# Kernel tuning notes

Measured on AMD Instinct MI355X. Metric: run time of the kernel, lower is better.

Reference implementation:

```python
import jax, jax.numpy as jnp
import numpy as np

DIM = 768
HEAD_DIM = 768


def setup_inputs() -> dict:
    key = jax.random.key(0)
    k_x, k_w, k_b = jax.random.split(key, 3)
    x = jax.random.normal(k_x, (4, 4096, DIM), dtype=jnp.float32)
    # torch Linear(dim, 3*head_dim): weight [3H, dim]; store transposed [dim, 3H]
    scale = 1.0 / np.sqrt(DIM)
    W_qkv = jax.random.uniform(k_w, (DIM, 3 * HEAD_DIM), dtype=jnp.float32,
                               minval=-scale, maxval=scale)
    b_qkv = jax.random.uniform(k_b, (3 * HEAD_DIM,), dtype=jnp.float32,
                               minval=-scale, maxval=scale)
    return {"x": x, "W_qkv": W_qkv, "b_qkv": b_qkv}


def reference(x, W_qkv, b_qkv):
    # x: [B, N, C]
    qkv = jnp.einsum("bnc,ch->bnh", x, W_qkv) + b_qkv  # [B, N, 3H]
    q, k, v = jnp.split(qkv, 3, axis=-1)               # each [B, N, H]
    H = q.shape[-1]
    scores = jnp.einsum("bnh,bmh->bnm", q, k) / jnp.sqrt(jnp.float32(H))
    attn = jax.nn.softmax(scores, axis=-1)             # [B, N, N]
    out = jnp.einsum("bnm,bmh->bnh", attn, v)          # [B, N, H]
    return out
```

## Files before the change

### kernel.cpp

```cpp
#include <hip/hip_runtime.h>
#include <stdint.h>

typedef __attribute__((ext_vector_type(8))) short short8;
typedef __attribute__((ext_vector_type(4))) float f32x4;

#define DIM 768
#define H3 2304
#define SEQ 4096
#define NTOK 16384

__device__ __forceinline__ unsigned short f2bf(float f) {
  union { float f; uint32_t u; } c; c.f = f;
  uint32_t u = c.u;
  u += 0x7FFFu + ((u >> 16) & 1u);
  return (unsigned short)(u >> 16);
}

__device__ __forceinline__ void async_cp16(const void* g, void* l) {
  __builtin_amdgcn_global_load_lds(
      (__attribute__((address_space(1))) void*)(void*)g,
      (__attribute__((address_space(3))) void*)l, 16, 0, 0);
}

#define MEMFENCE() asm volatile("" ::: "memory")
#define BARRIER() do { MEMFENCE(); __builtin_amdgcn_s_barrier(); MEMFENCE(); } while (0)
#define WAIT_VMCNT(n) asm volatile("s_waitcnt vmcnt(" #n ")" ::: "memory")

template <int N>
__device__ __forceinline__ void wait_lgk() {
  asm volatile("s_waitcnt lgkmcnt(%0)" :: "n"(N) : "memory");
  __builtin_amdgcn_sched_barrier(0);
}

template<int JN>
__device__ __forceinline__ void gemm_nt64_t(
    const unsigned short* __restrict__ A, const unsigned short* __restrict__ B,
    int K, int ldA, int ldB,
    unsigned short* As, unsigned short* Bs, f32x4 acc[4][JN])
{
  const int tid = threadIdx.x, lane = tid & 63, wid = tid >> 6;
  const int wm = (wid & 1) << 6, wn = (wid >> 1) * (JN * 16);
  const int lr = lane & 15, q = lane >> 4;

#pragma unroll
  for (int i = 0; i < 4; ++i)
#pragma unroll
    for (int j = 0; j < JN; ++j)
      acc[i][j] = (f32x4){0.f, 0.f, 0.f, 0.f};

  const unsigned short* gA[4];
  const unsigned short* gB[JN];
#pragma unroll
  for (int t = 0; t < 4; ++t) {
    const int c = tid + 256 * t;
    const int row = c >> 3, sc = c & 7;
    gA[t] = A + (size_t)row * ldA + (((sc ^ (row & 7)) << 3));
  }
#pragma unroll
  for (int t = 0; t < JN; ++t) {
    const int c = tid + 256 * t;
    const int row = c >> 3, sc = c & 7;
    gB[t] = B + (size_t)row * ldB + (((sc ^ (row & 7)) << 3));
  }

  for (int k0 = 0; k0 < K; k0 += 64) {
#pragma unroll
    for (int t = 0; t < 4; ++t)
      async_cp16(gA[t] + k0, As + (tid + 256 * t) * 8);
#pragma unroll
    for (int t = 0; t < JN; ++t)
      async_cp16(gB[t] + k0, Bs + (tid + 256 * t) * 8);
    __syncthreads();

    short8 af[4][2], bfr[JN][2];
#pragma unroll
    for (int i = 0; i < 4; ++i) {
      const int ra = wm + i * 16 + lr;
#pragma unroll
      for (int s2 = 0; s2 < 2; ++s2)
        af[i][s2] = *(const short8*)(As + ra * 64 + (((s2 * 4 + q) ^ (ra & 7)) << 3));
    }
#pragma unroll
    for (int j = 0; j < JN; ++j) {
      const int rb = wn + j * 16 + lr;
#pragma unroll
      for (int s2 = 0; s2 < 2; ++s2)
        bfr[j][s2] = *(const short8*)(Bs + rb * 64 + (((s2 * 4 + q) ^ (rb & 7)) << 3));
    }
#pragma unroll
    for (int s2 = 0; s2 < 2; ++s2)
#pragma unroll
      for (int i = 0; i < 4; ++i)
#pragma unroll
        for (int j = 0; j < JN; ++j)
          acc[i][j] = __builtin_amdgcn_mfma_f32_16x16x32_bf16(af[i][s2], bfr[j][s2], acc[i][j], 0, 0, 0);
    __syncthreads();
  }
}

template<int JN>
__device__ __forceinline__ void gemm256_nt(
    const unsigned short* __restrict__ A, const unsigned short* __restrict__ B,
    int K, int ldA, int ldB, unsigned short* lds, f32x4 acc[8][JN])
{
  constexpr int NB = JN - 2;
  const int tid = threadIdx.x, lane = tid & 63, wid = tid >> 6;
  const int wr = wid >> 2, wc = wid & 3;
  const int lr = lane & 15, q = lane >> 4;

  unsigned short* const As0 = lds;
  unsigned short* const As1 = lds + 16384;
  unsigned short* const Bs0 = lds + 32768;
  unsigned short* const Bs1 = lds + 32768 + JN * 4096;

#pragma unroll
  for (int i = 0; i < 8; ++i)
#pragma unroll
    for (int j = 0; j < JN; ++j)
      acc[i][j] = (f32x4){0.f, 0.f, 0.f, 0.f};

  const unsigned short* gA[4];
  const unsigned short* gB[JN];
#pragma unroll
  for (int t = 0; t < 4; ++t) {
    const int c = tid + 512 * t, row = c >> 3, sc = c & 7;
    gA[t] = A + (size_t)row * ldA + ((sc ^ (row & 7)) << 3);
  }
#pragma unroll
  for (int t = 0; t < JN; ++t) {
    const int c = tid + 512 * t, row = c >> 3, sc = c & 7;
    gB[t] = B + (size_t)row * ldB + ((sc ^ (row & 7)) << 3);
  }

  unsigned offA[8][2], offB[JN][2];
#pragma unroll
  for (int i = 0; i < 8; ++i) {
    const int ra = wr * 128 + i * 16 + lr;
#pragma unroll
    for (int h = 0; h < 2; ++h)
      offA[i][h] = ra * 64 + (((h * 4 + q) ^ (ra & 7)) << 3);
  }
#pragma unroll
  for (int j = 0; j < JN; ++j) {
    const int rb = wc * (JN * 16) + j * 16 + lr;
#pragma unroll
    for (int h = 0; h < 2; ++h)
      offB[j][h] = rb * 64 + (((h * 4 + q) ^ (rb & 7)) << 3);
  }

  const int nt = K >> 6;

#pragma unroll
  for (int t = 0; t < 4; ++t) async_cp16(gA[t], As0 + (tid + 512 * t) * 8);
#pragma unroll
  for (int t = 0; t < JN; ++t) async_cp16(gB[t], Bs0 + (tid + 512 * t) * 8);
  const int k1 = (nt > 1) ? 64 : 0;
#pragma unroll
  for (int t = 0; t < 4; ++t) async_cp16(gA[t] + k1, As1 + (tid + 512 * t) * 8);
  WAIT_VMCNT(4);
  BARRIER();

#pragma unroll 2
  for (int t = 0; t < nt; ++t) {
    const int p = t & 1;
    const unsigned short* const Asp = p ? As1 : As0;
    const unsigned short* const Bsp = p ? Bs1 : Bs0;
    unsigned short* const Bsn = p ? Bs0 : Bs1;
    unsigned short* const Asn = p ? As1 : As0;
    const int kB = ((t + 1 < nt) ? t + 1 : nt - 1) << 6;
    const int kA = ((t + 2 < nt) ? t + 2 : nt - 1) << 6;

#pragma unroll
    for (int u = 0; u < JN; ++u)
      async_cp16(gB[u] + kB, Bsn + (tid + 512 * u) * 8);

    short8 fa0[8], fa1[8], fbj[2], fbk[(NB > 0) ? NB : 1];
#pragma unroll
    for (int i = 0; i < 8; ++i) fa0[i] = *(const short8*)(Asp + offA[i][0]);
#pragma unroll
    for (int j = 0; j < 2; ++j) fbj[j] = *(const short8*)(Bsp + offB[j][0]);
#pragma unroll
    for (int j = 0; j < NB; ++j) fbk[j] = *(const short8*)(Bsp + offB[2 + j][0]);

    wait_lgk<NB>();
    __builtin_amdgcn_s_setprio(1);
#pragma unroll
    for (int i = 0; i < 8; ++i)
#pragma unroll
      for (int j = 0; j < 2; ++j)
        acc[i][j] = __builtin_amdgcn_mfma_f32_16x16x32_bf16(fa0[i], fbj[j], acc[i][j], 0, 0, 0);
    __builtin_amdgcn_s_setprio(0);

#pragma unroll
    for (int i = 0; i < 8; ++i) fa1[i] = *(const short8*)(Asp + offA[i][1]);
#pragma unroll
    for (int j = 0; j < 2; ++j) fbj[j] = *(const short8*)(Bsp + offB[j][1]);

    wait_lgk<10>();
    __builtin_amdgcn_s_setprio(1);
#pragma unroll
    for (int i = 0; i < 8; ++i)
#pragma unroll
      for (int j = 0; j < NB; ++j)
        acc[i][2 + j] = __builtin_amdgcn_mfma_f32_16x16x32_bf16(fa0[i], fbk[j], acc[i][2 + j], 0, 0, 0);
    __builtin_amdgcn_s_setprio(0);

#pragma unroll
    for (int j = 0; j < NB; ++j) fbk[j] = *(const short8*)(Bsp + offB[2 + j][1]);

    wait_lgk<NB>();
    __builtin_amdgcn_s_setprio(1);
#pragma unroll
    for (int i = 0; i < 8; ++i)
#pragma unroll
      for (int j = 0; j < 2; ++j)
        acc[i][j] = __builtin_amdgcn_mfma_f32_16x16x32_bf16(fa1[i], fbj[j], acc[i][j], 0, 0, 0);
    __builtin_amdgcn_s_setprio(0);

    BARRIER();
#pragma unroll
    for (int u = 0; u < 4; ++u)
      async_cp16(gA[u] + kA, Asn + (tid + 512 * u) * 8);

    wait_lgk<0>();
    __builtin_amdgcn_s_setprio(1);
#pragma unroll
    for (int i = 0; i < 8; ++i)
#pragma unroll
      for (int j = 0; j < NB; ++j)
        acc[i][2 + j] = __builtin_amdgcn_mfma_f32_16x16x32_bf16(fa1[i], fbk[j], acc[i][2 + j], 0, 0, 0);
    __builtin_amdgcn_s_setprio(0);

    WAIT_VMCNT(4);
    BARRIER();
  }
  WAIT_VMCNT(0);
  BARRIER();
}

__global__ __launch_bounds__(256) void k_cvt(const float* __restrict__ in,
                                             unsigned short* __restrict__ o) {
  int i = blockIdx.x * 256 + threadIdx.x;
  float4 f = ((const float4*)in)[i];
  ushort4 u;
  u.x = f2bf(f.x); u.y = f2bf(f.y); u.z = f2bf(f.z); u.w = f2bf(f.w);
  ((ushort4*)o)[i] = u;
}

__global__ __launch_bounds__(256) void k_transpose(const float* __restrict__ W,
                                                   unsigned short* __restrict__ Wt) {
  __shared__ float tile[32][33];
  const int bc = blockIdx.x * 32;
  const int br = blockIdx.y * 32;
  const int tx = threadIdx.x & 31, ty = threadIdx.x >> 5;
#pragma unroll
  for (int i = 0; i < 32; i += 8)
    tile[ty + i][tx] = W[(size_t)(br + ty + i) * H3 + bc + tx];
  __syncthreads();
#pragma unroll
  for (int i = 0; i < 32; i += 8)
    Wt[(size_t)(bc + ty + i) * DIM + br + tx] = f2bf(tile[tx][ty + i]);
}

__global__ __launch_bounds__(256) void k_qkv(
    const unsigned short* __restrict__ xbf, const unsigned short* __restrict__ Wt,
    const float* __restrict__ bias,
    unsigned short* __restrict__ qb, unsigned short* __restrict__ kb,
    unsigned short* __restrict__ vT)
{
  __shared__ unsigned short As[128 * 64];
  __shared__ unsigned short Bs[128 * 64];
  f32x4 acc[4][4];
  const int g = blockIdx.x;
  const int xcd = g & 7, slot = g >> 3;
  const int tn = slot % 18, grp = slot / 18;
  const int tm = xcd + 8 * grp;
  gemm_nt64_t<4>(xbf + (size_t)(tm * 128) * DIM, Wt + (size_t)(tn * 128) * DIM,
                 DIM, DIM, DIM, As, Bs, acc);

  const int tid = threadIdx.x, lane = tid & 63, wid = tid >> 6;
  const int wm = (wid & 1) << 6, wn = (wid >> 1) << 6;
  const float scale = 0.036084391824351615f;
#pragma unroll
  for (int i = 0; i < 4; ++i) {
#pragma unroll
    for (int j = 0; j < 4; ++j) {
      const int col  = tn * 128 + wn + j * 16 + (lane & 15);
      const int row0 = tm * 128 + wm + i * 16 + ((lane >> 4) << 2);
      const float bc = bias[col];
#pragma unroll
      for (int r = 0; r < 4; ++r) {
        const int row = row0 + r;
        const float v = acc[i][j][r] + bc;
        if (col < 768) {
          qb[(size_t)row * DIM + col] = f2bf(v * scale);
        } else if (col < 1536) {
          kb[(size_t)row * DIM + (col - 768)] = f2bf(v);
        } else {
          const int b = row >> 12, n = row & 4095;
          vT[((size_t)b * DIM + (col - 1536)) * SEQ + n] = f2bf(v);
        }
      }
    }
  }
}

__global__ __launch_bounds__(512, 2) void k_scores(
    const unsigned short* __restrict__ qb, const unsigned short* __restrict__ kb,
    unsigned short* __restrict__ S, float* __restrict__ lpart)
{
  __shared__ unsigned short lds[65536];
  f32x4 acc[8][4];
  const int g = blockIdx.x;
  const int xcd = g & 7, slot = g >> 3;
  const int grp = slot & 7, tn = slot >> 3;
  const int b  = xcd >> 1;
  const int ty = (grp << 1) | (xcd & 1);
  gemm256_nt<4>(qb + ((size_t)b * SEQ + ty * 256) * DIM,
                kb + ((size_t)b * SEQ + tn * 256) * DIM,
                DIM, DIM, DIM, lds, acc);

  const int tid = threadIdx.x, lane = tid & 63, wid = tid >> 6;
  const int wr = wid >> 2, wc = wid & 3;
  const int lr = lane & 15, q = lane >> 4;

  float rs[8][4];
#pragma unroll
  for (int i = 0; i < 8; ++i)
#pragma unroll
    for (int r = 0; r < 4; ++r) rs[i][r] = 0.f;

#pragma unroll
  for (int i = 0; i < 8; ++i)
#pragma unroll
    for (int j = 0; j < 4; ++j) {
      const int col = wc * 64 + j * 16 + lr;
#pragma unroll
      for (int r = 0; r < 4; ++r) {
        const int row = wr * 128 + i * 16 + (q << 2) + r;
        const float e = __expf(acc[i][j][r]);
        lds[row * 256 + (((col >> 3) ^ (((row >> 2) & 3) << 1)) << 3) + (col & 7)] = f2bf(e);
        rs[i][r] += e;
      }
    }

  float* lp = lpart + (size_t)(tn * 4 + wc) * NTOK;
  const int lbase = b * SEQ + ty * 256 + wr * 128 + (q << 2);
#pragma unroll
  for (int i = 0; i < 8; ++i)
#pragma unroll
    for (int r = 0; r < 4; ++r) {
      float v = rs[i][r];
      v += __shfl_xor(v, 1); v += __shfl_xor(v, 2);
      v += __shfl_xor(v, 4); v += __shfl_xor(v, 8);
      if (lr == 0) lp[lbase + i * 16 + r] = v;
    }
  __syncthreads();
  unsigned short* Sb = S + (size_t)b * SEQ * SEQ;
  const int rL = tid >> 5, cc = tid & 31;
#pragma unroll
  for (int pp = 0; pp < 16; ++pp) {
    const int row = pp * 16 + rL;
    const int pos = cc ^ (((row >> 2) & 3) << 1);
    *(uint4*)(Sb + (size_t)(ty * 256 + row) * SEQ + tn * 256 + cc * 8) =
        *(const uint4*)(lds + row * 256 + pos * 8);
  }
}

__global__ __launch_bounds__(256) void k_lred(const float* __restrict__ lpart,
                                              float* __restrict__ lsum) {
  const int tid = threadIdx.x;
  const int row = blockIdx.x * 64 + (tid >> 2);
  const int part = tid & 3;
  float s = 0.f;
#pragma unroll
  for (int t = 0; t < 16; ++t)
    s += lpart[(size_t)(part * 16 + t) * NTOK + row];
  s += __shfl_xor(s, 1);
  s += __shfl_xor(s, 2);
  if (part == 0) lsum[row] = 1.0f / s;
}

__global__ __launch_bounds__(512, 2) void k_pv(
    const unsigned short* __restrict__ P, const unsigned short* __restrict__ vT,
    const float* __restrict__ lsum, float* __restrict__ out)
{
  __shared__ unsigned short lds[57344];
  f32x4 acc[8][3];
  const int g = blockIdx.x;
  const int xcd = g & 7, s = g >> 3;
  const int combo = xcd * 2 + (s & 1);
  const int b = combo >> 2, tn = combo & 3;
  const int tm = s >> 1;
  gemm256_nt<3>(P + (size_t)b * SEQ * SEQ + (size_t)(tm * 256) * SEQ,
                vT + (size_t)b * DIM * SEQ + (size_t)(tn * 192) * SEQ,
                SEQ, SEQ, SEQ, lds, acc);

  const int tid = threadIdx.x, lane = tid & 63, wid = tid >> 6;
  const int wr = wid >> 2, wc = wid & 3;
  const int lr = lane & 15, q = lane >> 4;
  const int lbase = b * SEQ + tm * 256 + wr * 128 + (q << 2);
  float inv[8][4];
#pragma unroll
  for (int i = 0; i < 8; ++i)
#pragma unroll
    for (int r = 0; r < 4; ++r) inv[i][r] = lsum[lbase + i * 16 + r];
  float* ob = out + (size_t)b * SEQ * DIM;
#pragma unroll
  for (int i = 0; i < 8; ++i)
#pragma unroll
    for (int j = 0; j < 3; ++j) {
      const int col  = tn * 192 + wc * 48 + j * 16 + lr;
      const int row0 = tm * 256 + wr * 128 + i * 16 + (q << 2);
#pragma unroll
      for (int r = 0; r < 4; ++r)
        ob[(size_t)(row0 + r) * DIM + col] = acc[i][j][r] * inv[i][r];
    }
}

extern "C" void kernel_launch(void* const* d_in, const int* in_sizes, int n_in,
                              void* d_out, int out_size, void* d_ws, size_t ws_size,
                              hipStream_t stream) {
  const float* x    = (const float*)d_in[0];
  const float* W    = (const float*)d_in[1];
  const float* bias = (const float*)d_in[2];
  float* out = (float*)d_out;

  char* w = (char*)d_ws;
  unsigned short* x_bf = (unsigned short*)(w);
  unsigned short* Wt   = (unsigned short*)(w + 25165824);
  unsigned short* qb   = (unsigned short*)(w + 28704768);
  unsigned short* kb   = (unsigned short*)(w + 53870592);
  unsigned short* vT   = (unsigned short*)(w + 79036416);
  unsigned short* S    = (unsigned short*)(w + 104202240);
  float* lpart = (float*)(w);
  float* lsum  = (float*)(w + 4194304);

  k_cvt      <<<12288, 256, 0, stream>>>(x, x_bf);
  k_transpose<<<dim3(72, 24), 256, 0, stream>>>(W, Wt);
  k_qkv      <<<2304, 256, 0, stream>>>(x_bf, Wt, bias, qb, kb, vT);
  k_scores   <<<1024, 512, 0, stream>>>(qb, kb, S, lpart);
  k_lred     <<<256, 256, 0, stream>>>(lpart, lsum);
  k_pv       <<<256, 512, 0, stream>>>(S, vT, lsum, out);
}
```

Baseline: 422.0 us.

## Shrink scores kernel to 128x128 tiles with a new pipelined GEMM

Replaces the 256x256, 512-thread tile in the QK^T scores kernel with 128x128 tiles on 256-thread blocks, launching four times as many blocks. A new gemm128_nt routine double-buffers A and B in LDS with staggered async loads, split LDS waits and raised MFMA priority. The exp/row-sum epilogue and S write-out are remapped to the new tile, and the partial-sum layout still yields 64 parts. Smaller tiles cut per-block LDS and registers to raise occupancy and balance, at the cost of lower data reuse and more global reads of Q/K.

```diff
diff --git a/kernel.cpp b/kernel.cpp
--- a/kernel.cpp
+++ b/kernel.cpp
@@ -96,6 +96,111 @@
           acc[i][j] = __builtin_amdgcn_mfma_f32_16x16x32_bf16(af[i][s2], bfr[j][s2], acc[i][j], 0, 0, 0);
     __syncthreads();
   }
+}
+
+__device__ __forceinline__ void gemm128_nt(
+    const unsigned short* __restrict__ A, const unsigned short* __restrict__ B,
+    int K, int ldA, int ldB, unsigned short* lds, f32x4 acc[4][4])
+{
+  const int tid = threadIdx.x, lane = tid & 63, wid = tid >> 6;
+  const int wm = (wid & 1) << 6, wn = (wid >> 1) << 6;
+  const int lr = lane & 15, q = lane >> 4;
+
+  unsigned short* const As0 = lds;
+  unsigned short* const As1 = lds + 8192;
+  unsigned short* const Bs0 = lds + 16384;
+  unsigned short* const Bs1 = lds + 24576;
+
+#pragma unroll
+  for (int i = 0; i < 4; ++i)
+#pragma unroll
+    for (int j = 0; j < 4; ++j)
+      acc[i][j] = (f32x4){0.f, 0.f, 0.f, 0.f};
+
+  const unsigned short* gA[4];
+  const unsigned short* gB[4];
+#pragma unroll
+  for (int t = 0; t < 4; ++t) {
+    const int c = tid + 256 * t, row = c >> 3, sc = c & 7;
+    gA[t] = A + (size_t)row * ldA + ((sc ^ (row & 7)) << 3);
+    gB[t] = B + (size_t)row * ldB + ((sc ^ (row & 7)) << 3);
+  }
+
+  unsigned offA[4][2], offB[4][2];
+#pragma unroll
+  for (int i = 0; i < 4; ++i) {
+    const int ra = wm + i * 16 + lr;
+    const int rb = wn + i * 16 + lr;
+#pragma unroll
+    for (int h = 0; h < 2; ++h) {
+      offA[i][h] = ra * 64 + (((h * 4 + q) ^ (ra & 7)) << 3);
+      offB[i][h] = rb * 64 + (((h * 4 + q) ^ (rb & 7)) << 3);
+    }
+  }
+
+  const int nt = K >> 6;
+
+#pragma unroll
+  for (int t = 0; t < 4; ++t) async_cp16(gA[t], As0 + (tid + 256 * t) * 8);
+#pragma unroll
+  for (int t = 0; t < 4; ++t) async_cp16(gB[t], Bs0 + (tid + 256 * t) * 8);
+  const int k1 = (nt > 1) ? 64 : 0;
+#pragma unroll
+  for (int t = 0; t < 4; ++t) async_cp16(gA[t] + k1, As1 + (tid + 256 * t) * 8);
+  WAIT_VMCNT(4);
+  BARRIER();
+
+#pragma unroll 2
+  for (int t = 0; t < nt; ++t) {
+    const int p = t & 1;
+    const unsigned short* const Asp = p ? As1 : As0;
+    const unsigned short* const Bsp = p ? Bs1 : Bs0;
+    unsigned short* const Bsn = p ? Bs0 : Bs1;
+    unsigned short* const Asn = p ? As1 : As0;
+    const int kB = ((t + 1 < nt) ? t + 1 : nt - 1) << 6;
+    const int kA = ((t + 2 < nt) ? t + 2 : nt - 1) << 6;
+
+#pragma unroll
+    for (int u = 0; u < 4; ++u)
+      async_cp16(gB[u] + kB, Bsn + (tid + 256 * u) * 8);
+
+    short8 a0[4], b0[4], a1[4], b1[4];
+#pragma unroll
+    for (int i = 0; i < 4; ++i) a0[i] = *(const short8*)(Asp + offA[i][0]);
+#pragma unroll
+    for (int j = 0; j < 4; ++j) b0[j] = *(const short8*)(Bsp + offB[j][0]);
+#pragma unroll
+    for (int i = 0; i < 4; ++i) a1[i] = *(const short8*)(Asp + offA[i][1]);
+#pragma unroll
+    for (int j = 0; j < 4; ++j) b1[j] = *(const short8*)(Bsp + offB[j][1]);
+
+    wait_lgk<8>();
+    __builtin_amdgcn_s_setprio(1);
+#pragma unroll
+    for (int i = 0; i < 4; ++i)
+#pragma unroll
+      for (int j = 0; j < 4; ++j)
+        acc[i][j] = __builtin_amdgcn_mfma_f32_16x16x32_bf16(a0[i], b0[j], acc[i][j], 0, 0, 0);
+    __builtin_amdgcn_s_setprio(0);
+
+    wait_lgk<0>();
+    __builtin_amdgcn_s_setprio(1);
+#pragma unroll
+    for (int i = 0; i < 4; ++i)
+#pragma unroll
+      for (int j = 0; j < 4; ++j)
+        acc[i][j] = __builtin_amdgcn_mfma_f32_16x16x32_bf16(a1[i], b1[j], acc[i][j], 0, 0, 0);
+    __builtin_amdgcn_s_setprio(0);
+
+    BARRIER();
+#pragma unroll
+    for (int u = 0; u < 4; ++u)
+      async_cp16(gA[u] + kA, Asn + (tid + 256 * u) * 8);
+    WAIT_VMCNT(4);
+    BARRIER();
+  }
+  WAIT_VMCNT(0);
+  BARRIER();
 }
 
 template<int JN>
@@ -305,65 +410,64 @@
   }
 }
 
-__global__ __launch_bounds__(512, 2) void k_scores(
+__global__ __launch_bounds__(256, 2) void k_scores(
     const unsigned short* __restrict__ qb, const unsigned short* __restrict__ kb,
     unsigned short* __restrict__ S, float* __restrict__ lpart)
 {
-  __shared__ unsigned short lds[65536];
-  f32x4 acc[8][4];
+  __shared__ unsigned short lds[32768];
+  f32x4 acc[4][4];
   const int g = blockIdx.x;
   const int xcd = g & 7, slot = g >> 3;
-  const int grp = slot & 7, tn = slot >> 3;
+  const int grp = slot & 15, tn = slot >> 4;
   const int b  = xcd >> 1;
   const int ty = (grp << 1) | (xcd & 1);
-  gemm256_nt<4>(qb + ((size_t)b * SEQ + ty * 256) * DIM,
-                kb + ((size_t)b * SEQ + tn * 256) * DIM,
-                DIM, DIM, DIM, lds, acc);
+  gemm128_nt(qb + ((size_t)b * SEQ + ty * 128) * DIM,
+             kb + ((size_t)b * SEQ + tn * 128) * DIM,
+             DIM, DIM, DIM, lds, acc);
 
   const int tid = threadIdx.x, lane = tid & 63, wid = tid >> 6;
-  const int wr = wid >> 2, wc = wid & 3;
-  const int lr = lane & 15, q = lane >> 4;
-
-  float rs[8][4];
-#pragma unroll
-  for (int i = 0; i < 8; ++i)
+  const int wm = (wid & 1) << 6, wn = (wid >> 1) << 6;
+  const int q = lane >> 4;
+
+  float rs[4][4];
+#pragma unroll
+  for (int i = 0; i < 4; ++i) {
 #pragma unroll
     for (int r = 0; r < 4; ++r) rs[i][r] = 0.f;
-
-#pragma unroll
-  for (int i = 0; i < 8; ++i)
 #pragma unroll
     for (int j = 0; j < 4; ++j) {
-      const int col = wc * 64 + j * 16 + lr;
+      const int col = wn + j * 16 + (lane & 15);
 #pragma unroll
       for (int r = 0; r < 4; ++r) {
-        const int row = wr * 128 + i * 16 + (q << 2) + r;
+        const int row = wm + i * 16 + (q << 2) + r;
         const float e = __expf(acc[i][j][r]);
-        lds[row * 256 + (((col >> 3) ^ (((row >> 2) & 3) << 1)) << 3) + (col & 7)] = f2bf(e);
+        lds[row * 128 + (((col >> 3) ^ (((row >> 2) & 3) << 1)) << 3) + (col & 7)] = f2bf(e);
         rs[i][r] += e;
       }
     }
-
-  float* lp = lpart + (size_t)(tn * 4 + wc) * NTOK;
-  const int lbase = b * SEQ + ty * 256 + wr * 128 + (q << 2);
-#pragma unroll
-  for (int i = 0; i < 8; ++i)
+  }
+  const int half = wid >> 1;
+  const int lbase = b * SEQ + ty * 128 + wm + (q << 2);
+  float* lp = lpart + (size_t)(tn * 2 + half) * NTOK;
+#pragma unroll
+  for (int i = 0; i < 4; ++i)
 #pragma unroll
     for (int r = 0; r < 4; ++r) {
       float v = rs[i][r];
       v += __shfl_xor(v, 1); v += __shfl_xor(v, 2);
       v += __shfl_xor(v, 4); v += __shfl_xor(v, 8);
-      if (lr == 0) lp[lbase + i * 16 + r] = v;
+      if ((lane & 15) == 0)
+        lp[lbase + i * 16 + r] = v;
     }
   __syncthreads();
   unsigned short* Sb = S + (size_t)b * SEQ * SEQ;
-  const int rL = tid >> 5, cc = tid & 31;
-#pragma unroll
-  for (int pp = 0; pp < 16; ++pp) {
-    const int row = pp * 16 + rL;
+  const int rL = tid >> 4, cc = tid & 15;
+#pragma unroll
+  for (int p = 0; p < 8; ++p) {
+    const int row = p * 16 + rL;
     const int pos = cc ^ (((row >> 2) & 3) << 1);
-    *(uint4*)(Sb + (size_t)(ty * 256 + row) * SEQ + tn * 256 + cc * 8) =
-        *(const uint4*)(lds + row * 256 + pos * 8);
+    *(uint4*)(Sb + (size_t)(ty * 128 + row) * SEQ + tn * 128 + cc * 8) =
+        *(const uint4*)(lds + row * 128 + pos * 8);
   }
 }
 
@@ -439,7 +543,7 @@
   k_cvt      <<<12288, 256, 0, stream>>>(x, x_bf);
   k_transpose<<<dim3(72, 24), 256, 0, stream>>>(W, Wt);
   k_qkv      <<<2304, 256, 0, stream>>>(x_bf, Wt, bias, qb, kb, vT);
-  k_scores   <<<1024, 512, 0, stream>>>(qb, kb, S, lpart);
+  k_scores   <<<4096, 256, 0, stream>>>(qb, kb, S, lpart);
   k_lred     <<<256, 256, 0, stream>>>(lpart, lsum);
   k_pv       <<<256, 512, 0, stream>>>(S, vT, lsum, out);
 }
```

Result: slower. 451.2 us (+6.9%).
